# Performance work log

Measured on AMD Instinct MI355X. Metric: run time of the kernel, lower is better.

Reference implementation:

```python
import jax, jax.numpy as jnp
import numpy as np


def setup_inputs() -> dict:
    key = jax.random.key(0)
    B, C, A, P, N = 4, 1, 180, 384, 256
    sinogram = jax.random.normal(key, (B, C, A, P), dtype=jnp.float32)
    # projection angles uniformly covering [0, pi)
    thetas = jnp.linspace(0.0, np.pi, A, endpoint=False).astype(jnp.float32)
    # uniformly spaced detector positions centered at 0, unit spacing
    positions = jnp.arange(P, dtype=jnp.float32) - (P - 1) / 2.0
    return {"sinogram": sinogram, "thetas": thetas, "positions": positions, "image_size": N}


def reference(sinogram, thetas, positions, image_size):
    """Radon backprojection: image[y,x] = sum_a interp(sinogram[a], x*cos+y*sin)."""
    B, C, A, P = sinogram.shape
    N = image_size
    # pixel-center coordinates, image centered at origin (y axis pointing up)
    c = jnp.arange(N, dtype=sinogram.dtype) - (N - 1) / 2.0
    xs = c[None, :]          # [1, N]
    ys = -c[:, None]         # [N, 1]
    cos = jnp.cos(thetas)[:, None, None]  # [A, 1, 1]
    sin = jnp.sin(thetas)[:, None, None]
    t = xs[None] * cos + ys[None] * sin   # [A, N, N] detector coordinate per (angle, pixel)
    # fractional index into the (uniform) detector position grid
    dp = positions[1] - positions[0]
    f = (t - positions[0]) / dp           # [A, N, N]
    i0 = jnp.floor(f)
    w = f - i0                            # linear interpolation weight
    valid = (i0 >= 0) & (i0 <= P - 2)     # rays falling inside the detector
    i0c = jnp.clip(i0, 0, P - 2).astype(jnp.int32)
    idx = i0c.reshape(A, N * N)[None, None]          # [1, 1, A, N*N]
    v0 = jnp.take_along_axis(sinogram, idx, axis=3)  # [B, C, A, N*N]
    v1 = jnp.take_along_axis(sinogram, idx + 1, axis=3)
    wf = w.reshape(A, N * N)[None, None]
    vm = valid.reshape(A, N * N)[None, None]
    val = jnp.where(vm, v0 * (1.0 - wf) + v1 * wf, 0.0)
    return val.sum(axis=2).reshape(B, C, N, N)
```

## Files before the change

### kernel.cpp

```cpp
#include <hip/hip_runtime.h>
#include <hip/hip_fp16.h>
#include <cmath>


#define ACHUNKS 8

typedef __fp16 half2v __attribute__((ext_vector_type(2)));

__device__ __forceinline__ half2v as_h2(unsigned u) {
    union { unsigned u; half2v h; } x; x.u = u; return x.h;
}

__global__ __launch_bounds__(256) void radon_pack(
    const float* __restrict__ sino,
    const float* __restrict__ thetas,
    const float* __restrict__ positions,
    uint4* __restrict__ packed,
    float2* __restrict__ trig,
    int A, int P, int PES, int bstride)
{
    const int idx = blockIdx.x * 256 + threadIdx.x;
    const int a = idx / PES;
    const int j = idx - a * PES;
    if (a >= A) return;

    const float p0     = positions[0];
    const float inv_dp = 1.0f / (positions[1] - p0);
    if (j == 0) {
        float th = thetas[a];
        trig[a] = make_float2(cosf(th) * inv_dp, sinf(th) * inv_dp);
        if (a == 0) trig[A] = make_float2(-p0 * inv_dp, 0.0f);
    }

    uint4 e = make_uint4(0, 0, 0, 0);
    if (j >= 1 && j <= P - 1) {
        const float* s = sino + (size_t)a * P;
        unsigned* ep = (unsigned*)&e;
#pragma unroll
        for (int b = 0; b < 4; ++b) {
            const float* sb = s + (size_t)b * bstride;
            __half2 h = __floats2half2_rn(sb[j - 1], sb[j]);
            ep[b] = *(const unsigned*)&h;
        }
    }
    packed[(size_t)a * PES + j] = e;
}

__global__ __launch_bounds__(256) void radon_partial_pk(
    const uint4* __restrict__ packed,
    const float2* __restrict__ trig,
    float* __restrict__ part,
    int A, int P, int PES, int N, int chunk)
{
    const int tid = threadIdx.x;
    const int nn  = N * N;
    const int pix = blockIdx.x * 256 + tid;
    const int a0  = blockIdx.y * chunk;
    const int a1  = min(A, a0 + chunk);

    const int x = pix % N;
    const int y = pix / N;
    const float half = (float)(N - 1) * 0.5f;
    const float cx = (float)x - half;
    const float cy = half - (float)y;
    const float q0 = trig[A].x;

    float acc0 = 0.f, acc1 = 0.f, acc2 = 0.f, acc3 = 0.f;

#pragma unroll 4
    for (int a = a0; a < a1; ++a) {
        float2 t  = trig[a];
        float f   = fmaf(cx, t.x, fmaf(cy, t.y, q0));
        float i0f = floorf(f);
        float w   = f - i0f;
        int   i0  = (int)i0f;
        int   j   = min(max(i0, -1), P - 1) + 1;

        half2v w2 = __builtin_amdgcn_cvt_pkrtz(1.0f - w, w);
        uint4 e = packed[(size_t)a * PES + j];
        acc0 = __builtin_amdgcn_fdot2(as_h2(e.x), w2, acc0, false);
        acc1 = __builtin_amdgcn_fdot2(as_h2(e.y), w2, acc1, false);
        acc2 = __builtin_amdgcn_fdot2(as_h2(e.z), w2, acc2, false);
        acc3 = __builtin_amdgcn_fdot2(as_h2(e.w), w2, acc3, false);
    }

    if (pix < nn) {
        float* pp = part + (size_t)blockIdx.y * 4 * nn + pix;
        pp[0]              = acc0;
        pp[(size_t)nn]     = acc1;
        pp[(size_t)2 * nn] = acc2;
        pp[(size_t)3 * nn] = acc3;
    }
}

__global__ __launch_bounds__(256) void radon_reduce_kernel(
    const float4* __restrict__ part,
    float4* __restrict__ out,
    int BN4, int nchunks)
{
    int i = blockIdx.x * blockDim.x + threadIdx.x;
    if (i >= BN4) return;
    float4 s = make_float4(0.f, 0.f, 0.f, 0.f);
    for (int c = 0; c < nchunks; ++c) {
        float4 v = part[(size_t)c * BN4 + i];
        s.x += v.x; s.y += v.y; s.z += v.z; s.w += v.w;
    }
    out[i] = s;
}

__global__ __launch_bounds__(256) void radon_direct_kernel(
    const float* __restrict__ sino,
    const float* __restrict__ thetas,
    const float* __restrict__ positions,
    float* __restrict__ out,
    int A, int P, int N, int BC)
{
    const int nn  = N * N;
    const int pix = blockIdx.x * blockDim.x + threadIdx.x;
    if (pix >= nn) return;
    const float p0     = positions[0];
    const float inv_dp = 1.0f / (positions[1] - p0);
    const int x = pix % N;
    const int y = pix / N;
    const float half = (float)(N - 1) * 0.5f;
    const float cx = (float)x - half;
    const float cy = half - (float)y;
    for (int b = 0; b < BC; ++b) {
        float acc = 0.0f;
        for (int a = 0; a < A; ++a) {
            float th = thetas[a];
            float f  = (cx * cosf(th) + cy * sinf(th) - p0) * inv_dp;
            float i0f = floorf(f);
            int i0 = (int)i0f;
            float w = f - i0f;
            float m = (i0 >= 0 && i0 <= P - 2) ? 1.0f : 0.0f;
            int ic = min(max(i0, 0), P - 2);
            const float* row = sino + ((size_t)b * A + a) * P + ic;
            acc = fmaf(m, fmaf(w, row[1] - row[0], row[0]), acc);
        }
        out[(size_t)b * nn + pix] = acc;
    }
}

extern "C" void kernel_launch(void* const* d_in, const int* in_sizes, int n_in,
                              void* d_out, int out_size, void* d_ws, size_t ws_size,
                              hipStream_t stream) {
    const float* sino      = (const float*)d_in[0];
    const float* thetas    = (const float*)d_in[1];
    const float* positions = (const float*)d_in[2];
    float* out             = (float*)d_out;

    const int A  = in_sizes[1];
    const int P  = in_sizes[2];
    const int BC = in_sizes[0] / (A * P);
    const int N  = (int)lroundf(sqrtf((float)(out_size / BC)));
    const int nn = N * N;
    const int bstride = A * P;

    const int PES   = (P + 2 + 63) & ~63;
    const int chunk = (A + ACHUNKS - 1) / ACHUNKS;

    const size_t part_bytes   = (size_t)ACHUNKS * 4 * nn * sizeof(float);
    const size_t packed_bytes = (size_t)A * PES * sizeof(uint4);
    const size_t trig_bytes   = (size_t)(A + 1) * sizeof(float2);
    const size_t need = part_bytes + packed_bytes + trig_bytes;

    const bool fast = (BC == 4) && (A <= 1024) && (P >= 2)
                   && ((nn & 255) == 0) && ((nn & 3) == 0) && (ws_size >= need);

    if (fast) {
        float*  part   = (float*)d_ws;
        uint4*  packed = (uint4*)((char*)d_ws + part_bytes);
        float2* trig   = (float2*)((char*)d_ws + part_bytes + packed_bytes);

        dim3 block(256);
        dim3 gpack(((unsigned)(A * PES) + 255) / 256);
        radon_pack<<<gpack, block, 0, stream>>>(
            sino, thetas, positions, packed, trig, A, P, PES, bstride);

        dim3 gpart(nn / 256, ACHUNKS);
        radon_partial_pk<<<gpart, block, 0, stream>>>(
            packed, trig, part, A, P, PES, N, chunk);

        const int BN4 = nn;
        dim3 gred((BN4 + 255) / 256);
        radon_reduce_kernel<<<gred, block, 0, stream>>>(
            (const float4*)part, (float4*)out, BN4, ACHUNKS);
    } else {
        dim3 block(256);
        dim3 grid((nn + 255) / 256);
        radon_direct_kernel<<<grid, block, 0, stream>>>(
            sino, thetas, positions, out, A, P, N, BC);
    }
}
```

Baseline: 75.63 us.

## Fuse chunk reduction into partial kernel via last-block atomic counter

Removes the separate reduce kernel launch. Each partial block writes its partial sums, fences, and increments a per-pixel-block counter, and the last-arriving block over the angle chunks sums all partials and writes the output. The counters are zeroed inside the pack kernel, which also switches to float2 loads and the packed RTZ half conversion. This saves one launch and a global pass, but adds atomics, fences and a serialized tail read on the last block. The RTZ rounding also differs slightly from round-to-nearest.

```diff
diff --git a/kernel.cpp b/kernel.cpp
--- a/kernel.cpp
+++ b/kernel.cpp
@@ -17,11 +17,14 @@
     const float* __restrict__ positions,
     uint4* __restrict__ packed,
     float2* __restrict__ trig,
-    int A, int P, int PES, int bstride)
+    int* __restrict__ cnt,
+    int A, int P, int PES, int bstride, int nnb)
 {
-    const int idx = blockIdx.x * 256 + threadIdx.x;
-    const int a = idx / PES;
-    const int j = idx - a * PES;
+    const int gidx = blockIdx.x * 256 + threadIdx.x;
+    if (gidx < nnb) cnt[gidx] = 0;
+
+    const int a = gidx / PES;
+    const int j = gidx - a * PES;
     if (a >= A) return;
 
     const float p0     = positions[0];
@@ -34,28 +37,33 @@
 
     uint4 e = make_uint4(0, 0, 0, 0);
     if (j >= 1 && j <= P - 1) {
-        const float* s = sino + (size_t)a * P;
+        const float* s = sino + (size_t)a * P + (j - 1);
         unsigned* ep = (unsigned*)&e;
 #pragma unroll
         for (int b = 0; b < 4; ++b) {
-            const float* sb = s + (size_t)b * bstride;
-            __half2 h = __floats2half2_rn(sb[j - 1], sb[j]);
-            ep[b] = *(const unsigned*)&h;
+            float2 v = *(const float2*)(s + (size_t)b * bstride);
+            half2v h = __builtin_amdgcn_cvt_pkrtz(v.x, v.y);
+            union { half2v h; unsigned u; } cvt; cvt.h = h;
+            ep[b] = cvt.u;
         }
     }
     packed[(size_t)a * PES + j] = e;
 }
 
-__global__ __launch_bounds__(256) void radon_partial_pk(
+__global__ __launch_bounds__(256) void radon_partial_sk(
     const uint4* __restrict__ packed,
     const float2* __restrict__ trig,
     float* __restrict__ part,
+    int* __restrict__ cnt,
+    float* __restrict__ out,
     int A, int P, int PES, int N, int chunk)
 {
+    __shared__ int s_old;
     const int tid = threadIdx.x;
     const int nn  = N * N;
     const int pix = blockIdx.x * 256 + tid;
-    const int a0  = blockIdx.y * chunk;
+    const int c   = blockIdx.y;
+    const int a0  = c * chunk;
     const int a1  = min(A, a0 + chunk);
 
     const int x = pix % N;
@@ -84,28 +92,34 @@
         acc3 = __builtin_amdgcn_fdot2(as_h2(e.w), w2, acc3, false);
     }
 
-    if (pix < nn) {
-        float* pp = part + (size_t)blockIdx.y * 4 * nn + pix;
-        pp[0]              = acc0;
-        pp[(size_t)nn]     = acc1;
-        pp[(size_t)2 * nn] = acc2;
-        pp[(size_t)3 * nn] = acc3;
-    }
-}
-
-__global__ __launch_bounds__(256) void radon_reduce_kernel(
-    const float4* __restrict__ part,
-    float4* __restrict__ out,
-    int BN4, int nchunks)
-{
-    int i = blockIdx.x * blockDim.x + threadIdx.x;
-    if (i >= BN4) return;
-    float4 s = make_float4(0.f, 0.f, 0.f, 0.f);
-    for (int c = 0; c < nchunks; ++c) {
-        float4 v = part[(size_t)c * BN4 + i];
-        s.x += v.x; s.y += v.y; s.z += v.z; s.w += v.w;
-    }
-    out[i] = s;
+    float* pp = part + (size_t)c * 4 * nn + pix;
+    pp[0]              = acc0;
+    pp[(size_t)nn]     = acc1;
+    pp[(size_t)2 * nn] = acc2;
+    pp[(size_t)3 * nn] = acc3;
+
+    __threadfence();
+    __syncthreads();
+    if (tid == 0)
+        s_old = atomicAdd(&cnt[blockIdx.x], 1);
+    __syncthreads();
+    if (s_old == (int)gridDim.y - 1) {
+        __threadfence();
+        float r0 = 0.f, r1 = 0.f, r2 = 0.f, r3 = 0.f;
+#pragma unroll
+        for (int cc = 0; cc < ACHUNKS; ++cc) {
+            const float* qp = part + (size_t)cc * 4 * nn + pix;
+            r0 += qp[0];
+            r1 += qp[(size_t)nn];
+            r2 += qp[(size_t)2 * nn];
+            r3 += qp[(size_t)3 * nn];
+        }
+        float* op = out + pix;
+        op[0]              = r0;
+        op[(size_t)nn]     = r1;
+        op[(size_t)2 * nn] = r2;
+        op[(size_t)3 * nn] = r3;
+    }
 }
 
 __global__ __launch_bounds__(256) void radon_direct_kernel(
@@ -159,33 +173,32 @@
 
     const int PES   = (P + 2 + 63) & ~63;
     const int chunk = (A + ACHUNKS - 1) / ACHUNKS;
-
+    const int nnb   = nn / 256;
+
+    const size_t cnt_bytes    = ((size_t)nnb * sizeof(int) + 1023) & ~(size_t)1023;
     const size_t part_bytes   = (size_t)ACHUNKS * 4 * nn * sizeof(float);
     const size_t packed_bytes = (size_t)A * PES * sizeof(uint4);
     const size_t trig_bytes   = (size_t)(A + 1) * sizeof(float2);
-    const size_t need = part_bytes + packed_bytes + trig_bytes;
+    const size_t need = cnt_bytes + part_bytes + packed_bytes + trig_bytes;
 
     const bool fast = (BC == 4) && (A <= 1024) && (P >= 2)
-                   && ((nn & 255) == 0) && ((nn & 3) == 0) && (ws_size >= need);
+                   && ((nn & 255) == 0) && (ws_size >= need)
+                   && ((size_t)A * PES >= (size_t)nnb);
 
     if (fast) {
-        float*  part   = (float*)d_ws;
-        uint4*  packed = (uint4*)((char*)d_ws + part_bytes);
-        float2* trig   = (float2*)((char*)d_ws + part_bytes + packed_bytes);
+        int*    cnt    = (int*)d_ws;
+        float*  part   = (float*)((char*)d_ws + cnt_bytes);
+        uint4*  packed = (uint4*)((char*)d_ws + cnt_bytes + part_bytes);
+        float2* trig   = (float2*)((char*)d_ws + cnt_bytes + part_bytes + packed_bytes);
 
         dim3 block(256);
         dim3 gpack(((unsigned)(A * PES) + 255) / 256);
         radon_pack<<<gpack, block, 0, stream>>>(
-            sino, thetas, positions, packed, trig, A, P, PES, bstride);
+            sino, thetas, positions, packed, trig, cnt, A, P, PES, bstride, nnb);
 
         dim3 gpart(nn / 256, ACHUNKS);
-        radon_partial_pk<<<gpart, block, 0, stream>>>(
-            packed, trig, part, A, P, PES, N, chunk);
-
-        const int BN4 = nn;
-        dim3 gred((BN4 + 255) / 256);
-        radon_reduce_kernel<<<gred, block, 0, stream>>>(
-            (const float4*)part, (float4*)out, BN4, ACHUNKS);
+        radon_partial_sk<<<gpart, block, 0, stream>>>(
+            packed, trig, part, cnt, out, A, P, PES, N, chunk);
     } else {
         dim3 block(256);
         dim3 grid((nn + 255) / 256);
```

Result: slower. 249.1 us (+229.4%).
